# Kernel tuning notes

Hardware: AMD Instinct MI355X
Metric: run time of the kernel (lower is better)

Reference implementation:

```python
import jax, jax.numpy as jnp
import numpy as np

N = 64      # num_neighbors + 1
H = 512     # hidden_size
T = 1024    # history length


def setup_inputs() -> dict:
    key = jax.random.key(0)
    ks = jax.random.split(key, 10)
    s = 1.0 / np.sqrt(H)  # PyTorch LSTM/Linear init scale
    return {
        "in_recent_values": jax.random.normal(ks[0], (N,), dtype=jnp.float32),
        "in_reputation_history": jax.random.normal(ks[1], (N, T), dtype=jnp.float32),
        # per-module LSTM params (input_size=1), gate order i,f,g,o
        "W_ih": jax.random.uniform(ks[2], (N, 4 * H), jnp.float32, -s, s),      # [N,4H] (input_size=1 squeezed)
        "W_hh": jax.random.uniform(ks[3], (N, 4 * H, H), jnp.float32, -s, s),   # [N,4H,H]
        "b_ih": jax.random.uniform(ks[4], (N, 4 * H), jnp.float32, -s, s),
        "b_hh": jax.random.uniform(ks[5], (N, 4 * H), jnp.float32, -s, s),
        # per-module output Linear(H+1 -> 1)
        "lin_W": jax.random.uniform(ks[6], (N, H + 1), jnp.float32, -s, s),
        "lin_b": jax.random.uniform(ks[7], (N,), jnp.float32, -s, s),
        # final Linear(N -> 1)
        "final_W": jax.random.uniform(ks[8], (N,), jnp.float32, -1.0 / np.sqrt(N), 1.0 / np.sqrt(N)),
        "final_b": jax.random.uniform(ks[9], (1,), jnp.float32, -1.0 / np.sqrt(N), 1.0 / np.sqrt(N)),
    }


def _batched_lstm_last_h(history, W_ih, W_hh, b_ih, b_hh):
    # history: [N,T]. Precompute input contribution for all steps: [T,N,4H]
    x_proj = history[:, :, None] * W_ih[:, None, :] + (b_ih + b_hh)[:, None, :]
    x_proj = jnp.swapaxes(x_proj, 0, 1)  # [T,N,4H]

    def step(carry, x_t):
        h, c = carry  # [N,H] each
        gates = x_t + jnp.einsum("nh,ngh->ng", h, W_hh)  # [N,4H]
        i, f, g, o = jnp.split(gates, 4, axis=-1)
        i = jax.nn.sigmoid(i)
        f = jax.nn.sigmoid(f)
        g = jnp.tanh(g)
        o = jax.nn.sigmoid(o)
        c = f * c + i * g
        h = o * jnp.tanh(c)
        return (h, c), None

    h0 = jnp.zeros((N, H), dtype=history.dtype)
    (h_last, _), _ = jax.lax.scan(step, (h0, h0), x_proj)
    return h_last  # [N,H]


def reference(in_recent_values, in_reputation_history, W_ih, W_hh, b_ih, b_hh,
              lin_W, lin_b, final_W, final_b):
    h_last = _batched_lstm_last_h(in_reputation_history, W_ih, W_hh, b_ih, b_hh)
    # per-module linear on [h_last, current_reading] -> scalar each
    feat = jnp.concatenate([h_last, in_recent_values[:, None]], axis=1)  # [N,H+1]
    per_mod = jnp.sum(feat * lin_W, axis=1) + lin_b                      # [N]
    out = per_mod @ final_W + final_b                                    # [1]
    return out
```

## Files before the change

kernel.cpp:

```cpp
#include <hip/hip_runtime.h>
#include <hip/hip_fp16.h>
#include <cstddef>

#define NMOD 64
#define HID 512
#define TSTEPS 1024
#define G4 2048

#define WOFF_PERMOD 0
#define WOFF_HX     16384
#define WOFF_W16    524288
#define W16_BYTES   ((size_t)NMOD * G4 * HID * 2)
#define WS_NEED     (WOFF_W16 + W16_BYTES)

typedef _Float16 h2_t __attribute__((ext_vector_type(2)));
union U32H2 { unsigned u; h2_t h; };
__device__ __forceinline__ h2_t u2h(unsigned u) { U32H2 x; x.u = u; return x.h; }

#if __has_builtin(__builtin_amdgcn_fdot2)
#define FDOT2(a, b, c) __builtin_amdgcn_fdot2((a), (b), (c), false)
#else
__device__ __forceinline__ float FDOT2(h2_t a, h2_t b, float c) {
    return c + (float)a[0] * (float)b[0] + (float)a[1] * (float)b[1];
}
#endif

__device__ __forceinline__ float fsig(float x)  { return 1.0f / (1.0f + __expf(-x)); }
__device__ __forceinline__ float ftanh_(float x){ return 1.0f - 2.0f / (__expf(2.0f * x) + 1.0f); }

__global__ __launch_bounds__(256) void conv_kernel(const float* __restrict__ src,
                                                   __half* __restrict__ dst) {
    const size_t i = ((size_t)blockIdx.x * 256 + threadIdx.x) * 8;
    const float4 a = *reinterpret_cast<const float4*>(src + i);
    const float4 b = *reinterpret_cast<const float4*>(src + i + 4);
    __half2 h0 = __floats2half2_rn(a.x, a.y);
    __half2 h1 = __floats2half2_rn(a.z, a.w);
    __half2 h2 = __floats2half2_rn(b.x, b.y);
    __half2 h3 = __floats2half2_rn(b.z, b.w);
    uint4 o;
    o.x = *reinterpret_cast<unsigned*>(&h0);
    o.y = *reinterpret_cast<unsigned*>(&h1);
    o.z = *reinterpret_cast<unsigned*>(&h2);
    o.w = *reinterpret_cast<unsigned*>(&h3);
    *reinterpret_cast<uint4*>(dst + i) = o;
}

__global__ __launch_bounds__(512, 2) void lstm_res_kernel(
    const float* __restrict__ recent,
    const float* __restrict__ history,
    const float* __restrict__ W_ih,
    const float* __restrict__ b_ih,
    const float* __restrict__ b_hh,
    const float* __restrict__ lin_W,
    const float* __restrict__ lin_b,
    const unsigned* __restrict__ w16u,
    unsigned long long* hx,
    float* __restrict__ per_mod)
{
    const int bid = blockIdx.x;
    const int m = (bid & 7) * 8 + ((bid >> 3) >> 2);
    const int b = (bid >> 3) & 3;
    const int tid = threadIdx.x;
    const int rg = tid >> 4;
    const int cg = tid & 15;

    __shared__ unsigned w_lds[32768];
    __shared__ unsigned h_pk[256];
    __shared__ float gates_sh[512];
    __shared__ float hist_sh[TSTEPS];
    __shared__ float red_sh[8];

    for (int i = tid; i < TSTEPS; i += 512)
        hist_sh[i] = history[(size_t)m * TSTEPS + i];

    const size_t rowbase = (size_t)m * G4 * 256;
    uint4 w[12][4];
    #pragma unroll
    for (int r = 0; r < 12; ++r) {
        const int l = rg * 16 + r;
        const int gr = ((l >> 7) << 9) + (b << 7) + (l & 127);
        const uint4* src = (const uint4*)(w16u + rowbase + (size_t)gr * 256 + cg * 16);
        #pragma unroll
        for (int kk = 0; kk < 4; ++kk) w[r][kk] = src[kk];
    }
    #pragma unroll
    for (int r2 = 0; r2 < 4; ++r2) {
        const int l = rg * 16 + 12 + r2;
        const int gr = ((l >> 7) << 9) + (b << 7) + (l & 127);
        const uint4* src = (const uint4*)(w16u + rowbase + (size_t)gr * 256 + cg * 16);
        #pragma unroll
        for (int kk = 0; kk < 4; ++kk) {
            const int c = (cg * 4 + kk + rg) & 63;
            *(uint4*)&w_lds[((rg * 4 + r2) * 64 + c) * 4] = src[kk];
        }
    }

    const int rev = ((cg & 1) << 3) | ((cg & 2) << 1) | ((cg & 4) >> 1) | ((cg & 8) >> 3);
    const int l_own = rg * 16 + rev;
    const int gr_own = ((l_own >> 7) << 9) + (b << 7) + (l_own & 127);
    const float wib_own  = W_ih[(size_t)m * G4 + gr_own];
    const float bias_own = b_ih[(size_t)m * G4 + gr_own] + b_hh[(size_t)m * G4 + gr_own];

    if (tid < 256) h_pk[tid] = 0u;
    float c0 = 0.0f, c1 = 0.0f;
    __syncthreads();

    for (int t = 0; t < TSTEPS; ++t) {
        const float xv = hist_sh[t];
        float acc[16];
        #pragma unroll
        for (int r = 0; r < 16; ++r) acc[r] = 0.0f;

        #pragma unroll
        for (int kk = 0; kk < 4; ++kk) {
            const uint4 hq = *(const uint4*)&h_pk[(cg * 4 + kk) * 4];
            #pragma unroll
            for (int r = 0; r < 12; ++r) {
                acc[r] = FDOT2(u2h(w[r][kk].x), u2h(hq.x), acc[r]);
                acc[r] = FDOT2(u2h(w[r][kk].y), u2h(hq.y), acc[r]);
                acc[r] = FDOT2(u2h(w[r][kk].z), u2h(hq.z), acc[r]);
                acc[r] = FDOT2(u2h(w[r][kk].w), u2h(hq.w), acc[r]);
            }
            #pragma unroll
            for (int r2 = 0; r2 < 4; ++r2) {
                const int c = (cg * 4 + kk + rg) & 63;
                const uint4 lw = *(const uint4*)&w_lds[((rg * 4 + r2) * 64 + c) * 4];
                acc[12 + r2] = FDOT2(u2h(lw.x), u2h(hq.x), acc[12 + r2]);
                acc[12 + r2] = FDOT2(u2h(lw.y), u2h(hq.y), acc[12 + r2]);
                acc[12 + r2] = FDOT2(u2h(lw.z), u2h(hq.z), acc[12 + r2]);
                acc[12 + r2] = FDOT2(u2h(lw.w), u2h(hq.w), acc[12 + r2]);
            }
        }

        #pragma unroll
        for (int k = 0; k < 8; ++k) {
            const float send = (cg & 1) ? acc[k] : acc[8 + k];
            const float recv = __shfl_xor(send, 1, 64);
            acc[k] = ((cg & 1) ? acc[8 + k] : acc[k]) + recv;
        }
        #pragma unroll
        for (int k = 0; k < 4; ++k) {
            const float send = (cg & 2) ? acc[k] : acc[4 + k];
            const float recv = __shfl_xor(send, 2, 64);
            acc[k] = ((cg & 2) ? acc[4 + k] : acc[k]) + recv;
        }
        #pragma unroll
        for (int k = 0; k < 2; ++k) {
            const float send = (cg & 4) ? acc[k] : acc[2 + k];
            const float recv = __shfl_xor(send, 4, 64);
            acc[k] = ((cg & 4) ? acc[2 + k] : acc[k]) + recv;
        }
        {
            const float send = (cg & 8) ? acc[0] : acc[1];
            const float recv = __shfl_xor(send, 8, 64);
            acc[0] = ((cg & 8) ? acc[1] : acc[0]) + recv;
        }

        gates_sh[l_own] = acc[0] + xv * wib_own + bias_own;
        __syncthreads();

        const unsigned seq = (unsigned)(t + 1);
        const size_t pbase = (size_t)(seq & 1) * (NMOD * 256) + (size_t)m * 256;

        if (tid < 64) {
            const int e0 = 2 * tid, e1 = 2 * tid + 1;
            const float gi0 = fsig(gates_sh[e0]);
            const float gf0 = fsig(gates_sh[128 + e0]);
            const float gg0 = ftanh_(gates_sh[256 + e0]);
            const float go0 = fsig(gates_sh[384 + e0]);
            c0 = gf0 * c0 + gi0 * gg0;
            const float h0 = go0 * ftanh_(c0);
            const float gi1 = fsig(gates_sh[e1]);
            const float gf1 = fsig(gates_sh[128 + e1]);
            const float gg1 = ftanh_(gates_sh[256 + e1]);
            const float go1 = fsig(gates_sh[384 + e1]);
            c1 = gf1 * c1 + gi1 * gg1;
            const float h1 = go1 * ftanh_(c1);
            __half2 hh = __floats2half2_rn(h0, h1);
            const unsigned pay = *reinterpret_cast<unsigned*>(&hh);
            const unsigned long long v = ((unsigned long long)seq << 32) | pay;
            __hip_atomic_store(&hx[pbase + b * 64 + tid], v,
                               __ATOMIC_RELAXED, __HIP_MEMORY_SCOPE_AGENT);
            h_pk[b * 64 + tid] = pay;
        } else if (tid < 256) {
            const int p_idx = (b * 64 + tid) & 255;
            const unsigned long long* ap = &hx[pbase + p_idx];
            unsigned long long v;
            do {
                v = __hip_atomic_load(ap, __ATOMIC_RELAXED, __HIP_MEMORY_SCOPE_AGENT);
            } while ((unsigned)(v >> 32) != seq);
            h_pk[p_idx] = (unsigned)v;
        }
        __syncthreads();
    }

    if (b == 0) {
        float v = 0.0f;
        if (tid < 256) {
            U32H2 u; u.u = h_pk[tid];
            const float* lwp = lin_W + (size_t)m * (HID + 1);
            v = (float)u.h[0] * lwp[2 * tid] + (float)u.h[1] * lwp[2 * tid + 1];
        }
        #pragma unroll
        for (int s2 = 32; s2; s2 >>= 1) v += __shfl_xor(v, s2, 64);
        if ((tid & 63) == 0) red_sh[tid >> 6] = v;
        __syncthreads();
        if (tid == 0) {
            float s = 0.0f;
            #pragma unroll
            for (int wv2 = 0; wv2 < 8; ++wv2) s += red_sh[wv2];
            s += recent[m] * lin_W[(size_t)m * (HID + 1) + HID] + lin_b[m];
            per_mod[m] = s;
        }
    }
}

__global__ __launch_bounds__(1024) void lstm_module_kernel(
    const float* __restrict__ recent,
    const float* __restrict__ history,
    const float* __restrict__ W_ih,
    const float* __restrict__ W_hh,
    const float* __restrict__ b_ih,
    const float* __restrict__ b_hh,
    const float* __restrict__ lin_W,
    const float* __restrict__ lin_b,
    float* __restrict__ per_mod)
{
    const int n = blockIdx.x;
    const int tid = threadIdx.x;

    __shared__ float h_sh[HID];
    __shared__ float gates_sh[G4];
    __shared__ float wib_sh[G4];
    __shared__ float bias_sh[G4];
    __shared__ float hist_sh[TSTEPS];

    for (int i = tid; i < G4; i += 1024) {
        wib_sh[i]  = W_ih[(size_t)n * G4 + i];
        bias_sh[i] = b_ih[(size_t)n * G4 + i] + b_hh[(size_t)n * G4 + i];
    }
    for (int i = tid; i < TSTEPS; i += 1024) hist_sh[i] = history[(size_t)n * TSTEPS + i];
    if (tid < HID) h_sh[tid] = 0.0f;
    float c_reg = 0.0f;
    __syncthreads();

    const int sub = tid & 15;
    const int rid = tid >> 4;
    const float* Wbase = W_hh + (size_t)n * G4 * HID;

    for (int t = 0; t < TSTEPS; ++t) {
        const float x = hist_sh[t];
        float hreg[32];
        #pragma unroll
        for (int j = 0; j < 8; ++j) {
            const float4 hv = *reinterpret_cast<const float4*>(&h_sh[sub * 4 + j * 64]);
            hreg[4 * j + 0] = hv.x; hreg[4 * j + 1] = hv.y;
            hreg[4 * j + 2] = hv.z; hreg[4 * j + 3] = hv.w;
        }
        for (int p = 0; p < 32; ++p) {
            const int r = p * 64 + rid;
            const float* wr = Wbase + (size_t)r * HID + sub * 4;
            float acc = 0.0f;
            #pragma unroll
            for (int j = 0; j < 8; ++j) {
                const float4 wv = *reinterpret_cast<const float4*>(wr + j * 64);
                acc += wv.x * hreg[4*j+0] + wv.y * hreg[4*j+1]
                     + wv.z * hreg[4*j+2] + wv.w * hreg[4*j+3];
            }
            acc += __shfl_xor(acc, 1, 64);
            acc += __shfl_xor(acc, 2, 64);
            acc += __shfl_xor(acc, 4, 64);
            acc += __shfl_xor(acc, 8, 64);
            if (sub == 0) gates_sh[r] = acc + x * wib_sh[r] + bias_sh[r];
        }
        __syncthreads();
        if (tid < HID) {
            const float ig = fsig(gates_sh[tid]);
            const float fg = fsig(gates_sh[HID + tid]);
            const float gg = ftanh_(gates_sh[2 * HID + tid]);
            const float og = fsig(gates_sh[3 * HID + tid]);
            c_reg = fg * c_reg + ig * gg;
            h_sh[tid] = og * ftanh_(c_reg);
        }
        __syncthreads();
    }

    if (tid < HID) {
        float v = h_sh[tid] * lin_W[(size_t)n * (HID + 1) + tid];
        #pragma unroll
        for (int m2 = 32; m2; m2 >>= 1) v += __shfl_xor(v, m2, 64);
        if ((tid & 63) == 0) gates_sh[tid >> 6] = v;
    }
    __syncthreads();
    if (tid == 0) {
        float s = 0.0f;
        #pragma unroll
        for (int w = 0; w < HID / 64; ++w) s += gates_sh[w];
        s += recent[n] * lin_W[(size_t)n * (HID + 1) + HID] + lin_b[n];
        per_mod[n] = s;
    }
}

__global__ void finish_kernel(const float* __restrict__ per_mod,
                              const float* __restrict__ final_W,
                              const float* __restrict__ final_b,
                              float* __restrict__ out)
{
    const int l = threadIdx.x;
    float v = per_mod[l] * final_W[l];
    #pragma unroll
    for (int m = 32; m; m >>= 1) v += __shfl_xor(v, m, 64);
    if (l == 0) out[0] = v + final_b[0];
}

extern "C" void kernel_launch(void* const* d_in, const int* in_sizes, int n_in,
                              void* d_out, int out_size, void* d_ws, size_t ws_size,
                              hipStream_t stream) {
    const float* recent  = (const float*)d_in[0];
    const float* history = (const float*)d_in[1];
    const float* W_ih    = (const float*)d_in[2];
    const float* W_hh    = (const float*)d_in[3];
    const float* b_ih    = (const float*)d_in[4];
    const float* b_hh    = (const float*)d_in[5];
    const float* lin_W   = (const float*)d_in[6];
    const float* lin_b   = (const float*)d_in[7];
    const float* final_W = (const float*)d_in[8];
    const float* final_b = (const float*)d_in[9];
    float* out = (float*)d_out;
    float* per_mod = (float*)d_ws;

    if (ws_size >= WS_NEED) {
        __half* w16 = (__half*)((char*)d_ws + WOFF_W16);
        unsigned long long* hx = (unsigned long long*)((char*)d_ws + WOFF_HX);

        hipMemsetAsync(d_ws, 0, WOFF_W16, stream);

        const int conv_blocks = (int)((size_t)NMOD * G4 * HID / 8 / 256);
        conv_kernel<<<conv_blocks, 256, 0, stream>>>(W_hh, w16);

        lstm_res_kernel<<<NMOD * 4, 512, 0, stream>>>(
            recent, history, W_ih, b_ih, b_hh, lin_W, lin_b,
            (const unsigned*)w16, hx, per_mod);
    } else {
        lstm_module_kernel<<<NMOD, 1024, 0, stream>>>(
            recent, history, W_ih, W_hh, b_ih, b_hh, lin_W, lin_b, per_mod);
    }
    finish_kernel<<<1, 64, 0, stream>>>(per_mod, final_W, final_b, out);
}
```

Measured before the change: 2.653 ms.

## Overlap local h-slice matvec with cross-block h exchange wait

Reorders the K dimension so each block first multiplies by its own locally produced quarter of h, and does this while the reader threads' atomic loads of the peer blocks' h slices are in flight. The spin-wait on peers is moved after that partial matvec, and the remaining three quarters are processed only after a second barrier. The loop is peeled so the gate activation runs at the top of each iteration, with a final epilogue step. This hides inter-block communication latency on the serial recurrence, at the cost of an extra barrier per step and more complex index remapping of weights in registers and LDS.

```diff
diff --git a/kernel.cpp b/kernel.cpp
--- a/kernel.cpp
+++ b/kernel.cpp
@@ -79,19 +79,22 @@
     for (int r = 0; r < 12; ++r) {
         const int l = rg * 16 + r;
         const int gr = ((l >> 7) << 9) + (b << 7) + (l & 127);
-        const uint4* src = (const uint4*)(w16u + rowbase + (size_t)gr * 256 + cg * 16);
-        #pragma unroll
-        for (int kk = 0; kk < 4; ++kk) w[r][kk] = src[kk];
+        #pragma unroll
+        for (int kk = 0; kk < 4; ++kk) {
+            const int c = (((b + kk) & 3) << 4) + cg;
+            w[r][kk] = *(const uint4*)(w16u + rowbase + (size_t)gr * 256 + c * 4);
+        }
     }
     #pragma unroll
     for (int r2 = 0; r2 < 4; ++r2) {
         const int l = rg * 16 + 12 + r2;
         const int gr = ((l >> 7) << 9) + (b << 7) + (l & 127);
-        const uint4* src = (const uint4*)(w16u + rowbase + (size_t)gr * 256 + cg * 16);
         #pragma unroll
         for (int kk = 0; kk < 4; ++kk) {
-            const int c = (cg * 4 + kk + rg) & 63;
-            *(uint4*)&w_lds[((rg * 4 + r2) * 64 + c) * 4] = src[kk];
+            const int c  = (((b + kk) & 3) << 4) + cg;
+            const int wc = (((kk + rg) & 3) << 4) + cg;
+            *(uint4*)&w_lds[((rg * 4 + r2) * 64 + wc) * 4] =
+                *(const uint4*)(w16u + rowbase + (size_t)gr * 256 + c * 4);
         }
     }
 
@@ -101,68 +104,22 @@
     const float wib_own  = W_ih[(size_t)m * G4 + gr_own];
     const float bias_own = b_ih[(size_t)m * G4 + gr_own] + b_hh[(size_t)m * G4 + gr_own];
 
-    if (tid < 256) h_pk[tid] = 0u;
+    const bool is_writer = (tid < 64);
+    const bool is_reader = (tid >= 64 && tid < 256);
+    const int  rr    = tid - 64;
+    const int  widx  = (((b + 1 + (rr >> 6)) & 3) << 6) + (rr & 63);
+
     float c0 = 0.0f, c1 = 0.0f;
-    __syncthreads();
-
-    for (int t = 0; t < TSTEPS; ++t) {
-        const float xv = hist_sh[t];
-        float acc[16];
-        #pragma unroll
-        for (int r = 0; r < 16; ++r) acc[r] = 0.0f;
-
-        #pragma unroll
-        for (int kk = 0; kk < 4; ++kk) {
-            const uint4 hq = *(const uint4*)&h_pk[(cg * 4 + kk) * 4];
-            #pragma unroll
-            for (int r = 0; r < 12; ++r) {
-                acc[r] = FDOT2(u2h(w[r][kk].x), u2h(hq.x), acc[r]);
-                acc[r] = FDOT2(u2h(w[r][kk].y), u2h(hq.y), acc[r]);
-                acc[r] = FDOT2(u2h(w[r][kk].z), u2h(hq.z), acc[r]);
-                acc[r] = FDOT2(u2h(w[r][kk].w), u2h(hq.w), acc[r]);
-            }
-            #pragma unroll
-            for (int r2 = 0; r2 < 4; ++r2) {
-                const int c = (cg * 4 + kk + rg) & 63;
-                const uint4 lw = *(const uint4*)&w_lds[((rg * 4 + r2) * 64 + c) * 4];
-                acc[12 + r2] = FDOT2(u2h(lw.x), u2h(hq.x), acc[12 + r2]);
-                acc[12 + r2] = FDOT2(u2h(lw.y), u2h(hq.y), acc[12 + r2]);
-                acc[12 + r2] = FDOT2(u2h(lw.z), u2h(hq.z), acc[12 + r2]);
-                acc[12 + r2] = FDOT2(u2h(lw.w), u2h(hq.w), acc[12 + r2]);
-            }
-        }
-
-        #pragma unroll
-        for (int k = 0; k < 8; ++k) {
-            const float send = (cg & 1) ? acc[k] : acc[8 + k];
-            const float recv = __shfl_xor(send, 1, 64);
-            acc[k] = ((cg & 1) ? acc[8 + k] : acc[k]) + recv;
-        }
-        #pragma unroll
-        for (int k = 0; k < 4; ++k) {
-            const float send = (cg & 2) ? acc[k] : acc[4 + k];
-            const float recv = __shfl_xor(send, 2, 64);
-            acc[k] = ((cg & 2) ? acc[4 + k] : acc[k]) + recv;
-        }
-        #pragma unroll
-        for (int k = 0; k < 2; ++k) {
-            const float send = (cg & 4) ? acc[k] : acc[2 + k];
-            const float recv = __shfl_xor(send, 4, 64);
-            acc[k] = ((cg & 4) ? acc[2 + k] : acc[k]) + recv;
-        }
-        {
-            const float send = (cg & 8) ? acc[0] : acc[1];
-            const float recv = __shfl_xor(send, 8, 64);
-            acc[0] = ((cg & 8) ? acc[1] : acc[0]) + recv;
-        }
-
-        gates_sh[l_own] = acc[0] + xv * wib_own + bias_own;
+
+    gates_sh[l_own] = hist_sh[0] * wib_own + bias_own;
+
+    for (int t = 0; t < TSTEPS - 1; ++t) {
         __syncthreads();
-
         const unsigned seq = (unsigned)(t + 1);
         const size_t pbase = (size_t)(seq & 1) * (NMOD * 256) + (size_t)m * 256;
 
-        if (tid < 64) {
+        unsigned long long pv = 0;
+        if (is_writer) {
             const int e0 = 2 * tid, e1 = 2 * tid + 1;
             const float gi0 = fsig(gates_sh[e0]);
             const float gf0 = fsig(gates_sh[128 + e0]);
@@ -178,39 +135,147 @@
             const float h1 = go1 * ftanh_(c1);
             __half2 hh = __floats2half2_rn(h0, h1);
             const unsigned pay = *reinterpret_cast<unsigned*>(&hh);
-            const unsigned long long v = ((unsigned long long)seq << 32) | pay;
-            __hip_atomic_store(&hx[pbase + b * 64 + tid], v,
+            __hip_atomic_store(&hx[pbase + b * 64 + tid],
+                               ((unsigned long long)seq << 32) | pay,
                                __ATOMIC_RELAXED, __HIP_MEMORY_SCOPE_AGENT);
             h_pk[b * 64 + tid] = pay;
-        } else if (tid < 256) {
-            const int p_idx = (b * 64 + tid) & 255;
-            const unsigned long long* ap = &hx[pbase + p_idx];
-            unsigned long long v;
-            do {
-                v = __hip_atomic_load(ap, __ATOMIC_RELAXED, __HIP_MEMORY_SCOPE_AGENT);
-            } while ((unsigned)(v >> 32) != seq);
-            h_pk[p_idx] = (unsigned)v;
+        } else if (is_reader) {
+            pv = __hip_atomic_load(&hx[pbase + widx],
+                                   __ATOMIC_RELAXED, __HIP_MEMORY_SCOPE_AGENT);
         }
         __syncthreads();
-    }
-
-    if (b == 0) {
-        float v = 0.0f;
-        if (tid < 256) {
-            U32H2 u; u.u = h_pk[tid];
-            const float* lwp = lin_W + (size_t)m * (HID + 1);
-            v = (float)u.h[0] * lwp[2 * tid] + (float)u.h[1] * lwp[2 * tid + 1];
-        }
-        #pragma unroll
-        for (int s2 = 32; s2; s2 >>= 1) v += __shfl_xor(v, s2, 64);
-        if ((tid & 63) == 0) red_sh[tid >> 6] = v;
+
+        float acc[16];
+        #pragma unroll
+        for (int r = 0; r < 16; ++r) acc[r] = 0.0f;
+        {
+            const uint4 hq = *(const uint4*)&h_pk[(b << 6) + cg * 4];
+            #pragma unroll
+            for (int r = 0; r < 12; ++r) {
+                acc[r] = FDOT2(u2h(w[r][0].x), u2h(hq.x), acc[r]);
+                acc[r] = FDOT2(u2h(w[r][0].y), u2h(hq.y), acc[r]);
+                acc[r] = FDOT2(u2h(w[r][0].z), u2h(hq.z), acc[r]);
+                acc[r] = FDOT2(u2h(w[r][0].w), u2h(hq.w), acc[r]);
+            }
+            const int wc0 = ((rg & 3) << 4) + cg;
+            #pragma unroll
+            for (int r2 = 0; r2 < 4; ++r2) {
+                const uint4 lw = *(const uint4*)&w_lds[((rg * 4 + r2) * 64 + wc0) * 4];
+                acc[12 + r2] = FDOT2(u2h(lw.x), u2h(hq.x), acc[12 + r2]);
+                acc[12 + r2] = FDOT2(u2h(lw.y), u2h(hq.y), acc[12 + r2]);
+                acc[12 + r2] = FDOT2(u2h(lw.z), u2h(hq.z), acc[12 + r2]);
+                acc[12 + r2] = FDOT2(u2h(lw.w), u2h(hq.w), acc[12 + r2]);
+            }
+        }
+
+        if (is_reader) {
+            while ((unsigned)(pv >> 32) != seq)
+                pv = __hip_atomic_load(&hx[pbase + widx],
+                                       __ATOMIC_RELAXED, __HIP_MEMORY_SCOPE_AGENT);
+            h_pk[widx] = (unsigned)pv;
+        }
         __syncthreads();
-        if (tid == 0) {
-            float s = 0.0f;
-            #pragma unroll
-            for (int wv2 = 0; wv2 < 8; ++wv2) s += red_sh[wv2];
-            s += recent[m] * lin_W[(size_t)m * (HID + 1) + HID] + lin_b[m];
-            per_mod[m] = s;
+
+        #pragma unroll
+        for (int kk = 1; kk < 4; ++kk) {
+            const uint4 hq = *(const uint4*)&h_pk[((((b + kk) & 3)) << 6) + cg * 4];
+            #pragma unroll
+            for (int r = 0; r < 12; ++r) {
+                acc[r] = FDOT2(u2h(w[r][kk].x), u2h(hq.x), acc[r]);
+                acc[r] = FDOT2(u2h(w[r][kk].y), u2h(hq.y), acc[r]);
+                acc[r] = FDOT2(u2h(w[r][kk].z), u2h(hq.z), acc[r]);
+                acc[r] = FDOT2(u2h(w[r][kk].w), u2h(hq.w), acc[r]);
+            }
+            const int wc = (((kk + rg) & 3) << 4) + cg;
+            #pragma unroll
+            for (int r2 = 0; r2 < 4; ++r2) {
+                const uint4 lw = *(const uint4*)&w_lds[((rg * 4 + r2) * 64 + wc) * 4];
+                acc[12 + r2] = FDOT2(u2h(lw.x), u2h(hq.x), acc[12 + r2]);
+                acc[12 + r2] = FDOT2(u2h(lw.y), u2h(hq.y), acc[12 + r2]);
+                acc[12 + r2] = FDOT2(u2h(lw.z), u2h(hq.z), acc[12 + r2]);
+                acc[12 + r2] = FDOT2(u2h(lw.w), u2h(hq.w), acc[12 + r2]);
+            }
+        }
+
+        #pragma unroll
+        for (int k = 0; k < 8; ++k) {
+            const float send = (cg & 1) ? acc[k] : acc[8 + k];
+            const float recv = __shfl_xor(send, 1, 64);
+            acc[k] = ((cg & 1) ? acc[8 + k] : acc[k]) + recv;
+        }
+        #pragma unroll
+        for (int k = 0; k < 4; ++k) {
+            const float send = (cg & 2) ? acc[k] : acc[4 + k];
+            const float recv = __shfl_xor(send, 2, 64);
+            acc[k] = ((cg & 2) ? acc[4 + k] : acc[k]) + recv;
+        }
+        #pragma unroll
+        for (int k = 0; k < 2; ++k) {
+            const float send = (cg & 4) ? acc[k] : acc[2 + k];
+            const float recv = __shfl_xor(send, 4, 64);
+            acc[k] = ((cg & 4) ? acc[2 + k] : acc[k]) + recv;
+        }
+        {
+            const float send = (cg & 8) ? acc[0] : acc[1];
+            const float recv = __shfl_xor(send, 8, 64);
+            acc[0] = ((cg & 8) ? acc[1] : acc[0]) + recv;
+        }
+
+        gates_sh[l_own] = acc[0] + hist_sh[t + 1] * wib_own + bias_own;
+    }
+
+    __syncthreads();
+    {
+        const unsigned seq = (unsigned)TSTEPS;
+        const size_t pbase = (size_t)(seq & 1) * (NMOD * 256) + (size_t)m * 256;
+        if (is_writer) {
+            const int e0 = 2 * tid, e1 = 2 * tid + 1;
+            const float gi0 = fsig(gates_sh[e0]);
+            const float gf0 = fsig(gates_sh[128 + e0]);
+            const float gg0 = ftanh_(gates_sh[256 + e0]);
+            const float go0 = fsig(gates_sh[384 + e0]);
+            c0 = gf0 * c0 + gi0 * gg0;
+            const float h0 = go0 * ftanh_(c0);
+            const float gi1 = fsig(gates_sh[e1]);
+            const float gf1 = fsig(gates_sh[128 + e1]);
+            const float gg1 = ftanh_(gates_sh[256 + e1]);
+            const float go1 = fsig(gates_sh[384 + e1]);
+            c1 = gf1 * c1 + gi1 * gg1;
+            const float h1 = go1 * ftanh_(c1);
+            __half2 hh = __floats2half2_rn(h0, h1);
+            const unsigned pay = *reinterpret_cast<unsigned*>(&hh);
+            __hip_atomic_store(&hx[pbase + b * 64 + tid],
+                               ((unsigned long long)seq << 32) | pay,
+                               __ATOMIC_RELAXED, __HIP_MEMORY_SCOPE_AGENT);
+            h_pk[b * 64 + tid] = pay;
+        }
+        if (b == 0) {
+            if (is_reader) {
+                unsigned long long pv;
+                do {
+                    pv = __hip_atomic_load(&hx[pbase + widx],
+                                           __ATOMIC_RELAXED, __HIP_MEMORY_SCOPE_AGENT);
+                } while ((unsigned)(pv >> 32) != seq);
+                h_pk[widx] = (unsigned)pv;
+            }
+            __syncthreads();
+            float v = 0.0f;
+            if (tid < 256) {
+                U32H2 u; u.u = h_pk[tid];
+                const float* lwp = lin_W + (size_t)m * (HID + 1);
+                v = (float)u.h[0] * lwp[2 * tid] + (float)u.h[1] * lwp[2 * tid + 1];
+            }
+            #pragma unroll
+            for (int s2 = 32; s2; s2 >>= 1) v += __shfl_xor(v, s2, 64);
+            if ((tid & 63) == 0) red_sh[tid >> 6] = v;
+            __syncthreads();
+            if (tid == 0) {
+                float s = 0.0f;
+                #pragma unroll
+                for (int wv2 = 0; wv2 < 8; ++wv2) s += red_sh[wv2];
+                s += recent[m] * lin_W[(size_t)m * (HID + 1) + HID] + lin_b[m];
+                per_mod[m] = s;
+            }
         }
     }
 }
```

Measured after the change: 2.587 ms. -2.5%, faster.

## Split LSTM recurrence by hidden columns and exchange partial gate sums

Applied to the files above, without the earlier changes.

Each of the four blocks per module now holds a 128-column slice of W_hh for all 2048 gate rows. It computes partial dot products for every gate, then exchanges fp32 partial sums with its peers through sequence-tagged global slots, so every block ends up with its own 128 hidden units. This drops the separate fp16 conversion kernel, since weights are packed to fp16 directly at load, and it replaces the cross-lane shuffles with DPP moves. The trade is more traffic per step: each block sends three times 512 partial sums instead of 64 packed h values. It also moves the final linear-layer combine into finish_kernel, and the memset now always covers the exchange buffer.

```diff
diff --git a/kernel.cpp b/kernel.cpp
--- a/kernel.cpp
+++ b/kernel.cpp
@@ -8,10 +8,9 @@
 #define G4 2048
 
 #define WOFF_PERMOD 0
-#define WOFF_HX     16384
-#define WOFF_W16    524288
-#define W16_BYTES   ((size_t)NMOD * G4 * HID * 2)
-#define WS_NEED     (WOFF_W16 + W16_BYTES)
+#define WOFF_HX     8192
+#define HX_WORDS    (2ull * NMOD * 4 * 4 * 512)
+#define WS_NEED     (WOFF_HX + HX_WORDS * 8ull)
 
 typedef _Float16 h2_t __attribute__((ext_vector_type(2)));
 union U32H2 { unsigned u; h2_t h; };
@@ -28,203 +27,197 @@
 __device__ __forceinline__ float fsig(float x)  { return 1.0f / (1.0f + __expf(-x)); }
 __device__ __forceinline__ float ftanh_(float x){ return 1.0f - 2.0f / (__expf(2.0f * x) + 1.0f); }
 
-__global__ __launch_bounds__(256) void conv_kernel(const float* __restrict__ src,
-                                                   __half* __restrict__ dst) {
-    const size_t i = ((size_t)blockIdx.x * 256 + threadIdx.x) * 8;
-    const float4 a = *reinterpret_cast<const float4*>(src + i);
-    const float4 b = *reinterpret_cast<const float4*>(src + i + 4);
+template<int CTRL>
+__device__ __forceinline__ float dppf(float x) {
+    int xi = __builtin_bit_cast(int, x);
+    int r = __builtin_amdgcn_update_dpp(0, xi, CTRL, 0xF, 0xF, true);
+    return __builtin_bit_cast(float, r);
+}
+
+__device__ __forceinline__ uint4 pack8(const float* p) {
+    const float4 a = *reinterpret_cast<const float4*>(p);
+    const float4 c = *reinterpret_cast<const float4*>(p + 4);
     __half2 h0 = __floats2half2_rn(a.x, a.y);
     __half2 h1 = __floats2half2_rn(a.z, a.w);
-    __half2 h2 = __floats2half2_rn(b.x, b.y);
-    __half2 h3 = __floats2half2_rn(b.z, b.w);
+    __half2 h2 = __floats2half2_rn(c.x, c.y);
+    __half2 h3 = __floats2half2_rn(c.z, c.w);
     uint4 o;
     o.x = *reinterpret_cast<unsigned*>(&h0);
     o.y = *reinterpret_cast<unsigned*>(&h1);
     o.z = *reinterpret_cast<unsigned*>(&h2);
     o.w = *reinterpret_cast<unsigned*>(&h3);
-    *reinterpret_cast<uint4*>(dst + i) = o;
-}
-
-__global__ __launch_bounds__(512, 2) void lstm_res_kernel(
-    const float* __restrict__ recent,
-    const float* __restrict__ history,
-    const float* __restrict__ W_ih,
-    const float* __restrict__ b_ih,
-    const float* __restrict__ b_hh,
-    const float* __restrict__ lin_W,
-    const float* __restrict__ lin_b,
-    const unsigned* __restrict__ w16u,
-    unsigned long long* hx,
-    float* __restrict__ per_mod)
-{
-    const int bid = blockIdx.x;
-    const int m = (bid & 7) * 8 + ((bid >> 3) >> 2);
-    const int b = (bid >> 3) & 3;
-    const int tid = threadIdx.x;
-    const int rg = tid >> 4;
-    const int cg = tid & 15;
-
-    __shared__ unsigned w_lds[32768];
-    __shared__ unsigned h_pk[256];
-    __shared__ float gates_sh[512];
-    __shared__ float hist_sh[TSTEPS];
-    __shared__ float red_sh[8];
-
-    for (int i = tid; i < TSTEPS; i += 512)
-        hist_sh[i] = history[(size_t)m * TSTEPS + i];
-
-    const size_t rowbase = (size_t)m * G4 * 256;
-    uint4 w[12][4];
-    #pragma unroll
-    for (int r = 0; r < 12; ++r) {
-        const int l = rg * 16 + r;
-        const int gr = ((l >> 7) << 9) + (b << 7) + (l & 127);
-        const uint4* src = (const uint4*)(w16u + rowbase + (size_t)gr * 256 + cg * 16);
-        #pragma unroll
-        for (int kk = 0; kk < 4; ++kk) w[r][kk] = src[kk];
-    }
-    #pragma unroll
-    for (int r2 = 0; r2 < 4; ++r2) {
-        const int l = rg * 16 + 12 + r2;
-        const int gr = ((l >> 7) << 9) + (b << 7) + (l & 127);
-        const uint4* src = (const uint4*)(w16u + rowbase + (size_t)gr * 256 + cg * 16);
-        #pragma unroll
-        for (int kk = 0; kk < 4; ++kk) {
-            const int c = (cg * 4 + kk + rg) & 63;
-            *(uint4*)&w_lds[((rg * 4 + r2) * 64 + c) * 4] = src[kk];
-        }
-    }
-
-    const int rev = ((cg & 1) << 3) | ((cg & 2) << 1) | ((cg & 4) >> 1) | ((cg & 8) >> 3);
-    const int l_own = rg * 16 + rev;
-    const int gr_own = ((l_own >> 7) << 9) + (b << 7) + (l_own & 127);
-    const float wib_own  = W_ih[(size_t)m * G4 + gr_own];
-    const float bias_own = b_ih[(size_t)m * G4 + gr_own] + b_hh[(size_t)m * G4 + gr_own];
-
-    if (tid < 256) h_pk[tid] = 0u;
-    float c0 = 0.0f, c1 = 0.0f;
-    __syncthreads();
-
-    for (int t = 0; t < TSTEPS; ++t) {
-        const float xv = hist_sh[t];
-        float acc[16];
-        #pragma unroll
-        for (int r = 0; r < 16; ++r) acc[r] = 0.0f;
-
-        #pragma unroll
-        for (int kk = 0; kk < 4; ++kk) {
-            const uint4 hq = *(const uint4*)&h_pk[(cg * 4 + kk) * 4];
-            #pragma unroll
-            for (int r = 0; r < 12; ++r) {
-                acc[r] = FDOT2(u2h(w[r][kk].x), u2h(hq.x), acc[r]);
-                acc[r] = FDOT2(u2h(w[r][kk].y), u2h(hq.y), acc[r]);
-                acc[r] = FDOT2(u2h(w[r][kk].z), u2h(hq.z), acc[r]);
-                acc[r] = FDOT2(u2h(w[r][kk].w), u2h(hq.w), acc[r]);
-            }
-            #pragma unroll
-            for (int r2 = 0; r2 < 4; ++r2) {
-                const int c = (cg * 4 + kk + rg) & 63;
-                const uint4 lw = *(const uint4*)&w_lds[((rg * 4 + r2) * 64 + c) * 4];
-                acc[12 + r2] = FDOT2(u2h(lw.x), u2h(hq.x), acc[12 + r2]);
-                acc[12 + r2] = FDOT2(u2h(lw.y), u2h(hq.y), acc[12 + r2]);
-                acc[12 + r2] = FDOT2(u2h(lw.z), u2h(hq.z), acc[12 + r2]);
-                acc[12 + r2] = FDOT2(u2h(lw.w), u2h(hq.w), acc[12 + r2]);
-            }
-        }
-
-        #pragma unroll
-        for (int k = 0; k < 8; ++k) {
-            const float send = (cg & 1) ? acc[k] : acc[8 + k];
-            const float recv = __shfl_xor(send, 1, 64);
-            acc[k] = ((cg & 1) ? acc[8 + k] : acc[k]) + recv;
-        }
-        #pragma unroll
-        for (int k = 0; k < 4; ++k) {
-            const float send = (cg & 2) ? acc[k] : acc[4 + k];
-            const float recv = __shfl_xor(send, 2, 64);
-            acc[k] = ((cg & 2) ? acc[4 + k] : acc[k]) + recv;
-        }
-        #pragma unroll
-        for (int k = 0; k < 2; ++k) {
-            const float send = (cg & 4) ? acc[k] : acc[2 + k];
-            const float recv = __shfl_xor(send, 4, 64);
-            acc[k] = ((cg & 4) ? acc[2 + k] : acc[k]) + recv;
-        }
-        {
-            const float send = (cg & 8) ? acc[0] : acc[1];
-            const float recv = __shfl_xor(send, 8, 64);
-            acc[0] = ((cg & 8) ? acc[1] : acc[0]) + recv;
-        }
-
-        gates_sh[l_own] = acc[0] + xv * wib_own + bias_own;
-        __syncthreads();
-
-        const unsigned seq = (unsigned)(t + 1);
-        const size_t pbase = (size_t)(seq & 1) * (NMOD * 256) + (size_t)m * 256;
-
-        if (tid < 64) {
-            const int e0 = 2 * tid, e1 = 2 * tid + 1;
-            const float gi0 = fsig(gates_sh[e0]);
-            const float gf0 = fsig(gates_sh[128 + e0]);
-            const float gg0 = ftanh_(gates_sh[256 + e0]);
-            const float go0 = fsig(gates_sh[384 + e0]);
-            c0 = gf0 * c0 + gi0 * gg0;
-            const float h0 = go0 * ftanh_(c0);
-            const float gi1 = fsig(gates_sh[e1]);
-            const float gf1 = fsig(gates_sh[128 + e1]);
-            const float gg1 = ftanh_(gates_sh[256 + e1]);
-            const float go1 = fsig(gates_sh[384 + e1]);
-            c1 = gf1 * c1 + gi1 * gg1;
-            const float h1 = go1 * ftanh_(c1);
-            __half2 hh = __floats2half2_rn(h0, h1);
-            const unsigned pay = *reinterpret_cast<unsigned*>(&hh);
-            const unsigned long long v = ((unsigned long long)seq << 32) | pay;
-            __hip_atomic_store(&hx[pbase + b * 64 + tid], v,
-                               __ATOMIC_RELAXED, __HIP_MEMORY_SCOPE_AGENT);
-            h_pk[b * 64 + tid] = pay;
-        } else if (tid < 256) {
-            const int p_idx = (b * 64 + tid) & 255;
-            const unsigned long long* ap = &hx[pbase + p_idx];
-            unsigned long long v;
-            do {
-                v = __hip_atomic_load(ap, __ATOMIC_RELAXED, __HIP_MEMORY_SCOPE_AGENT);
-            } while ((unsigned)(v >> 32) != seq);
-            h_pk[p_idx] = (unsigned)v;
-        }
-        __syncthreads();
-    }
-
-    if (b == 0) {
-        float v = 0.0f;
-        if (tid < 256) {
-            U32H2 u; u.u = h_pk[tid];
-            const float* lwp = lin_W + (size_t)m * (HID + 1);
-            v = (float)u.h[0] * lwp[2 * tid] + (float)u.h[1] * lwp[2 * tid + 1];
-        }
-        #pragma unroll
-        for (int s2 = 32; s2; s2 >>= 1) v += __shfl_xor(v, s2, 64);
-        if ((tid & 63) == 0) red_sh[tid >> 6] = v;
-        __syncthreads();
-        if (tid == 0) {
-            float s = 0.0f;
-            #pragma unroll
-            for (int wv2 = 0; wv2 < 8; ++wv2) s += red_sh[wv2];
-            s += recent[m] * lin_W[(size_t)m * (HID + 1) + HID] + lin_b[m];
-            per_mod[m] = s;
-        }
-    }
-}
-
-__global__ __launch_bounds__(1024) void lstm_module_kernel(
-    const float* __restrict__ recent,
+    return o;
+}
+
+__device__ __forceinline__ float dot4(uint4 wv, uint4 hv, float acc) {
+    acc = FDOT2(u2h(wv.x), u2h(hv.x), acc);
+    acc = FDOT2(u2h(wv.y), u2h(hv.y), acc);
+    acc = FDOT2(u2h(wv.z), u2h(hv.z), acc);
+    acc = FDOT2(u2h(wv.w), u2h(hv.w), acc);
+    return acc;
+}
+
+__global__ __launch_bounds__(512, 2) void lstm_col_kernel(
     const float* __restrict__ history,
     const float* __restrict__ W_ih,
     const float* __restrict__ W_hh,
     const float* __restrict__ b_ih,
     const float* __restrict__ b_hh,
     const float* __restrict__ lin_W,
-    const float* __restrict__ lin_b,
-    float* __restrict__ per_mod)
+    unsigned long long* hx,
+    float* __restrict__ per_mod4)
+{
+    const int bid = blockIdx.x;
+    const int m = (bid & 7) * 8 + (bid >> 5);
+    const int b = (bid >> 3) & 3;
+    const int tid = threadIdx.x;
+    const int rg = tid >> 4;
+    const int cg = tid & 15;
+
+    __shared__ unsigned w_lds[32768];
+    __shared__ float part_lds[512];
+    __shared__ float gates_sh[512];
+    __shared__ unsigned h_u32[64];
+    __shared__ float hist_sh[TSTEPS];
+    __shared__ float red_sh[8];
+
+    for (int i = tid; i < TSTEPS; i += 512)
+        hist_sh[i] = history[(size_t)m * TSTEPS + i];
+    if (tid < 64) h_u32[tid] = 0u;
+
+    const float* wmB = W_hh + (size_t)m * G4 * HID + (size_t)(b * 128 + cg * 8);
+    uint4 w[3][16];
+    #pragma unroll
+    for (int Q = 0; Q < 3; ++Q)
+        #pragma unroll
+        for (int u = 0; u < 16; ++u)
+            w[Q][u] = pack8(wmB + (size_t)(rg * 64 + Q * 16 + u) * HID);
+    #pragma unroll
+    for (int u = 0; u < 16; ++u)
+        *(uint4*)&w_lds[((rg * 16 + u) * 16 + cg) * 4] =
+            pack8(wmB + (size_t)(rg * 64 + 48 + u) * HID);
+
+    const int gri = (tid >> 7) * 512 + b * 128 + (tid & 127);
+    const float wib_i  = W_ih[(size_t)m * G4 + gri];
+    const float bias_i = b_ih[(size_t)m * G4 + gri] + b_hh[(size_t)m * G4 + gri];
+
+    const int rev = ((cg & 1) << 3) | ((cg & 2) << 1) | ((cg & 4) >> 1) | ((cg & 8) >> 3);
+    const int ob  = (rg >> 1) & 3;
+    const bool own = (ob == b);
+    const int drb = ((rg >> 3) << 7) + ((rg & 1) << 6) + rev;
+    const int s0 = (b + 1) & 3, s1 = (b + 2) & 3, s2 = (b + 3) & 3;
+
+    float c_reg = 0.0f;
+    __syncthreads();
+
+    for (int t = 0; t < TSTEPS; ++t) {
+        const unsigned seq = (unsigned)(t + 1);
+        unsigned long long* hxp = hx + ((size_t)(seq & 1) * NMOD + m) * (4 * 4 * 512);
+
+        const uint4 hq = *(const uint4*)&h_u32[cg * 4];
+        #pragma unroll
+        for (int Q = 0; Q < 4; ++Q) {
+            float acc[16];
+            #pragma unroll
+            for (int u = 0; u < 16; ++u) {
+                uint4 wv;
+                if (Q < 3) wv = w[Q][u];
+                else       wv = *(const uint4*)&w_lds[((rg * 16 + u) * 16 + cg) * 4];
+                acc[u] = dot4(wv, hq, 0.0f);
+            }
+            #pragma unroll
+            for (int k = 0; k < 8; ++k) {
+                const float send = (cg & 1) ? acc[k] : acc[8 + k];
+                const float recv = dppf<0xB1>(send);
+                acc[k] = ((cg & 1) ? acc[8 + k] : acc[k]) + recv;
+            }
+            #pragma unroll
+            for (int k = 0; k < 4; ++k) {
+                const float send = (cg & 2) ? acc[k] : acc[4 + k];
+                const float recv = dppf<0x4E>(send);
+                acc[k] = ((cg & 2) ? acc[4 + k] : acc[k]) + recv;
+            }
+            #pragma unroll
+            for (int k = 0; k < 2; ++k) {
+                const float send = (cg & 4) ? acc[k] : acc[2 + k];
+                const float recv = dppf<0x141>(send);
+                acc[k] = ((cg & 4) ? acc[2 + k] : acc[k]) + recv;
+            }
+            {
+                const float send = (cg & 8) ? acc[0] : acc[1];
+                const float recv = dppf<0x140>(send);
+                acc[0] = ((cg & 8) ? acc[1] : acc[0]) + recv;
+            }
+            const float S = acc[0];
+            const int dr = drb + Q * 16;
+            if (own) {
+                part_lds[dr] = S;
+            } else {
+                __hip_atomic_store(&hxp[(size_t)(ob * 4 + b) * 512 + dr],
+                                   ((unsigned long long)seq << 32) |
+                                   (unsigned long long)__float_as_uint(S),
+                                   __ATOMIC_RELAXED, __HIP_MEMORY_SCOPE_AGENT);
+            }
+        }
+
+        unsigned long long* a0 = &hxp[(size_t)(b * 4 + s0) * 512 + tid];
+        unsigned long long* a1 = &hxp[(size_t)(b * 4 + s1) * 512 + tid];
+        unsigned long long* a2 = &hxp[(size_t)(b * 4 + s2) * 512 + tid];
+        unsigned long long v0 = __hip_atomic_load(a0, __ATOMIC_RELAXED, __HIP_MEMORY_SCOPE_AGENT);
+        unsigned long long v1 = __hip_atomic_load(a1, __ATOMIC_RELAXED, __HIP_MEMORY_SCOPE_AGENT);
+        unsigned long long v2 = __hip_atomic_load(a2, __ATOMIC_RELAXED, __HIP_MEMORY_SCOPE_AGENT);
+        __syncthreads();
+
+        float sum = part_lds[tid];
+        while ((unsigned)(v0 >> 32) != seq)
+            v0 = __hip_atomic_load(a0, __ATOMIC_RELAXED, __HIP_MEMORY_SCOPE_AGENT);
+        while ((unsigned)(v1 >> 32) != seq)
+            v1 = __hip_atomic_load(a1, __ATOMIC_RELAXED, __HIP_MEMORY_SCOPE_AGENT);
+        while ((unsigned)(v2 >> 32) != seq)
+            v2 = __hip_atomic_load(a2, __ATOMIC_RELAXED, __HIP_MEMORY_SCOPE_AGENT);
+        sum += __uint_as_float((unsigned)v0);
+        sum += __uint_as_float((unsigned)v1);
+        sum += __uint_as_float((unsigned)v2);
+        const float g = sum + hist_sh[t] * wib_i + bias_i;
+        gates_sh[tid] = ((tid >> 7) == 2) ? ftanh_(g) : fsig(g);
+        __syncthreads();
+
+        if (tid < 128) {
+            const float gi = gates_sh[tid];
+            const float gf = gates_sh[128 + tid];
+            const float gg = gates_sh[256 + tid];
+            const float go = gates_sh[384 + tid];
+            c_reg = gf * c_reg + gi * gg;
+            ((__half*)h_u32)[tid] = __float2half(go * ftanh_(c_reg));
+        }
+        __syncthreads();
+    }
+
+    float v = 0.0f;
+    if (tid < 128) {
+        const float hvf = __half2float(((const __half*)h_u32)[tid]);
+        v = hvf * lin_W[(size_t)m * (HID + 1) + b * 128 + tid];
+    }
+    #pragma unroll
+    for (int sft = 32; sft; sft >>= 1) v += __shfl_xor(v, sft, 64);
+    if ((tid & 63) == 0) red_sh[tid >> 6] = v;
+    __syncthreads();
+    if (tid == 0) {
+        float s = 0.0f;
+        #pragma unroll
+        for (int wv2 = 0; wv2 < 8; ++wv2) s += red_sh[wv2];
+        per_mod4[m * 4 + b] = s;
+    }
+}
+
+__global__ __launch_bounds__(1024) void lstm_module_kernel(
+    const float* __restrict__ history,
+    const float* __restrict__ W_ih,
+    const float* __restrict__ W_hh,
+    const float* __restrict__ b_ih,
+    const float* __restrict__ b_hh,
+    const float* __restrict__ lin_W,
+    float* __restrict__ per_mod4)
 {
     const int n = blockIdx.x;
     const int tid = threadIdx.x;
@@ -296,18 +289,23 @@
         float s = 0.0f;
         #pragma unroll
         for (int w = 0; w < HID / 64; ++w) s += gates_sh[w];
-        s += recent[n] * lin_W[(size_t)n * (HID + 1) + HID] + lin_b[n];
-        per_mod[n] = s;
-    }
-}
-
-__global__ void finish_kernel(const float* __restrict__ per_mod,
+        per_mod4[n * 4] = s;
+    }
+}
+
+__global__ void finish_kernel(const float* __restrict__ per_mod4,
+                              const float* __restrict__ recent,
+                              const float* __restrict__ lin_W,
+                              const float* __restrict__ lin_b,
                               const float* __restrict__ final_W,
                               const float* __restrict__ final_b,
                               float* __restrict__ out)
 {
     const int l = threadIdx.x;
-    float v = per_mod[l] * final_W[l];
+    float s = per_mod4[l * 4 + 0] + per_mod4[l * 4 + 1]
+            + per_mod4[l * 4 + 2] + per_mod4[l * 4 + 3]
+            + recent[l] * lin_W[(size_t)l * (HID + 1) + HID] + lin_b[l];
+    float v = s * final_W[l];
     #pragma unroll
     for (int m = 32; m; m >>= 1) v += __shfl_xor(v, m, 64);
     if (l == 0) out[0] = v + final_b[0];
@@ -327,23 +325,18 @@
     const float* final_W = (const float*)d_in[8];
     const float* final_b = (const float*)d_in[9];
     float* out = (float*)d_out;
-    float* per_mod = (float*)d_ws;
+    float* per_mod4 = (float*)d_ws;
+
+    hipMemsetAsync(d_ws, 0, WS_NEED, stream);
 
     if (ws_size >= WS_NEED) {
-        __half* w16 = (__half*)((char*)d_ws + WOFF_W16);
         unsigned long long* hx = (unsigned long long*)((char*)d_ws + WOFF_HX);
-
-        hipMemsetAsync(d_ws, 0, WOFF_W16, stream);
-
-        const int conv_blocks = (int)((size_t)NMOD * G4 * HID / 8 / 256);
-        conv_kernel<<<conv_blocks, 256, 0, stream>>>(W_hh, w16);
-
-        lstm_res_kernel<<<NMOD * 4, 512, 0, stream>>>(
-            recent, history, W_ih, b_ih, b_hh, lin_W, lin_b,
-            (const unsigned*)w16, hx, per_mod);
+        lstm_col_kernel<<<NMOD * 4, 512, 0, stream>>>(
+            history, W_ih, W_hh, b_ih, b_hh, lin_W, hx, per_mod4);
     } else {
         lstm_module_kernel<<<NMOD, 1024, 0, stream>>>(
-            recent, history, W_ih, W_hh, b_ih, b_hh, lin_W, lin_b, per_mod);
-    }
-    finish_kernel<<<1, 64, 0, stream>>>(per_mod, final_W, final_b, out);
-}
+            history, W_ih, W_hh, b_ih, b_hh, lin_W, per_mod4);
+    }
+    finish_kernel<<<1, 64, 0, stream>>>(per_mod4, recent, lin_W, lin_b,
+                                        final_W, final_b, out);
+}
```

Result: slower. 4.002 ms (+50.9%).
